# Optimization experiments

Hardware: AMD Instinct MI355X
Metric: run time of the kernel (lower is better)

## Reference

```python
import jax, jax.numpy as jnp
import numpy as np

N_ING, N_DIR = 100000, 50000
E = 1000000
H, D = 4, 16          # heads, per-head dim
HID = H * D           # 64
LAT, COND = 32, 8
F_ING, F_DIR = 16, 8
OUT_ING = 16


def _han_edge(x_src, x_dst, att_s, att_d, edge_index, n_dst):
    # HANConv per-edge-type attention message passing.
    src, dst = edge_index[0], edge_index[1]
    a = jax.nn.leaky_relu(
        jnp.einsum('nhd,hd->nh', x_src, att_s)[src]
        + jnp.einsum('nhd,hd->nh', x_dst, att_d)[dst],
        negative_slope=0.2)                               # [E, H]
    amax = jax.ops.segment_max(a, dst, num_segments=n_dst)
    ex = jnp.exp(a - amax[dst])
    denom = jax.ops.segment_sum(ex, dst, num_segments=n_dst)
    alpha = ex / (denom[dst] + 1e-16)                     # PyG softmax eps
    out = jax.ops.segment_sum(x_src[src] * alpha[:, :, None], dst,
                              num_segments=n_dst)         # [n_dst, H, D]
    return jax.nn.relu(out.reshape(n_dst, HID))


def _group(outs, q, Wk, bk):
    # HANConv semantic-level attention across edge types.
    s = jnp.stack(outs)                                   # [T, N, HID]
    score = jnp.tanh(s @ Wk + bk).mean(axis=1) @ q        # [T]
    attn = jax.nn.softmax(score)
    return jnp.einsum('t,tnf->nf', attn, s)


def setup_inputs() -> dict:
    key = jax.random.key(0)
    ks = jax.random.split(key, 32)
    def ei(k, n_src, n_dst):
        k1, k2 = jax.random.split(k)
        return jnp.stack([jax.random.randint(k1, (E,), 0, n_src),
                          jax.random.randint(k2, (E,), 0, n_dst)]).astype(jnp.int64)
    s = 0.1
    inp = {
        'x_ing': jax.random.normal(ks[0], (N_ING, F_ING), jnp.float32),
        'x_dir': jax.random.normal(ks[1], (N_DIR, F_DIR), jnp.float32),
        'cond':  jax.random.normal(ks[2], (COND,), jnp.float32),
        'eps':   jax.random.normal(ks[3], (1, LAT), jnp.float32),
        'ei_cooc':     ei(ks[4], N_ING, N_DIR),
        'ei_used':     ei(ks[5], N_ING, N_DIR),
        'ei_contains': ei(ks[6], N_DIR, N_ING),
        'ei_pairs':    ei(ks[7], N_DIR, N_DIR),
        'ei_follows':  ei(ks[8], N_DIR, N_DIR),
        # node-type projections
        'W_pi': jax.random.normal(ks[9],  (F_ING, HID)) * s,
        'b_pi': jnp.zeros((HID,)),
        'W_pd': jax.random.normal(ks[10], (F_DIR, HID)) * s,
        'b_pd': jnp.zeros((HID,)),
        # semantic attention
        'Wk': jax.random.normal(ks[21], (HID, HID)) * s,
        'bk': jnp.zeros((HID,)),
        'q':  jax.random.normal(ks[22], (HID,)) * s,
        # VAE heads (input: 2*HID + COND)
        'W_mu': jax.random.normal(ks[23], (2 * HID + COND, LAT)) * s,
        'b_mu': jnp.zeros((LAT,)),
        'W_lv': jax.random.normal(ks[24], (2 * HID + COND, LAT)) * s,
        'b_lv': jnp.zeros((LAT,)),
        # decoder (fc1 is dead code in the original forward)
        'W_fc3': jax.random.normal(ks[25], (LAT, HID)) * s,
        'b_fc3': jnp.zeros((HID,)),
        'W_fc2': jax.random.normal(ks[26], (HID, OUT_ING)) * s,
        'b_fc2': jnp.zeros((OUT_ING,)),
    }
    for i, name in enumerate(['cooc', 'used', 'contains', 'pairs', 'follows']):
        inp[f'as_{name}'] = jax.random.normal(ks[11 + i], (H, D)) * s
        inp[f'ad_{name}'] = jax.random.normal(ks[16 + i], (H, D)) * s
    return inp


def reference(x_ing, x_dir, cond, eps,
              ei_cooc, ei_used, ei_contains, ei_pairs, ei_follows,
              W_pi, b_pi, W_pd, b_pd,
              as_cooc, ad_cooc, as_used, ad_used, as_contains, ad_contains,
              as_pairs, ad_pairs, as_follows, ad_follows,
              Wk, bk, q, W_mu, b_mu, W_lv, b_lv,
              W_fc3, b_fc3, W_fc2, b_fc2):
    # node-type projections -> [N, H, D]
    h_ing = (x_ing @ W_pi + b_pi).reshape(N_ING, H, D)
    h_dir = (x_dir @ W_pd + b_pd).reshape(N_DIR, H, D)

    o_cooc = _han_edge(h_ing, h_dir, as_cooc, ad_cooc, ei_cooc, N_DIR)
    o_used = _han_edge(h_ing, h_dir, as_used, ad_used, ei_used, N_DIR)
    o_cont = _han_edge(h_dir, h_ing, as_contains, ad_contains, ei_contains, N_ING)
    o_pair = _han_edge(h_dir, h_dir, as_pairs, ad_pairs, ei_pairs, N_DIR)
    o_foll = _han_edge(h_dir, h_dir, as_follows, ad_follows, ei_follows, N_DIR)

    out_ing = _group([o_cont], q, Wk, bk)                       # [N_ING, HID]
    out_dir = _group([o_cooc, o_used, o_pair, o_foll], q, Wk, bk)

    ingre_pool = out_ing.mean(axis=0, keepdims=True)            # [1, HID]
    direc_pool = out_dir.mean(axis=0, keepdims=True)
    graph_repr = jnp.concatenate([ingre_pool, direc_pool, cond[None]], axis=1)

    mu = graph_repr @ W_mu + b_mu
    logvar = graph_repr @ W_lv + b_lv
    z = mu + eps * jnp.exp(0.5 * logvar)

    # decoder: fc1 branch is overwritten in the original; effective path below
    recon = jnp.tanh(jax.nn.relu(z @ W_fc3 + b_fc3) @ W_fc2 + b_fc2)  # [1, OUT_ING]
    return recon, mu, logvar
```

## Files before the change

kernel.cpp:

```cpp
#include <hip/hip_runtime.h>
#include <hip/hip_fp16.h>
#include <math.h>

#define N_ING 100000
#define N_DIR 50000
#define NE    1000000
#define NDST_TOTAL 300000
#define NBUCK 4688
#define BA    16
#define NBK   (5 * BA)
#define I4PT  (NE / 4)
#define PB_ING 384
#define PB_DIR 192

typedef float v2f __attribute__((ext_vector_type(2)));

__global__ __launch_bounds__(256) void kA_kernel(
    const int* __restrict__ e0, const int* __restrict__ e1,
    const int* __restrict__ e2, const int* __restrict__ e3,
    const int* __restrict__ e4, int* __restrict__ blockcnt,
    const float* __restrict__ x_ing, const float* __restrict__ W_pi,
    const float* __restrict__ b_pi,
    const float* __restrict__ as_cooc, const float* __restrict__ as_used,
    const float* __restrict__ ad_contains,
    unsigned* __restrict__ h8_ing, __half* __restrict__ s_ing,
    const float* __restrict__ x_dir, const float* __restrict__ W_pd,
    const float* __restrict__ b_pd,
    const float* __restrict__ ad_cooc, const float* __restrict__ ad_used,
    const float* __restrict__ as_contains, const float* __restrict__ as_pairs,
    const float* __restrict__ ad_pairs, const float* __restrict__ as_follows,
    const float* __restrict__ ad_follows,
    unsigned* __restrict__ h8_dir, __half* __restrict__ s_dir)
{
    __shared__ int hist[NBUCK];
    __shared__ float sW[16 * 64];
    __shared__ float sbb[64];
    __shared__ float satt[7 * 64];
    __shared__ float sx[4][16];
    __shared__ float srow[4][64];

    const int bid = blockIdx.x;
    const int tid = threadIdx.x;
    if (bid < NBK) {
        const int type = bid / BA, blk = bid % BA;
        const int* ei = type == 0 ? e0 : type == 1 ? e1 : type == 2 ? e2
                      : type == 3 ? e3 : e4;
        const int base = type == 0 ? 0 : type == 1 ? 50000 : type == 2 ? 100000
                       : type == 3 ? 200000 : 250000;
        for (int i = tid; i < NBUCK; i += 256) hist[i] = 0;
        __syncthreads();
        const int4* d4 = (const int4*)(ei + NE);
        for (int i = blk * 256 + tid; i < I4PT; i += BA * 256) {
            int4 d = d4[i];
            atomicAdd(&hist[(base + d.x) >> 6], 1);
            atomicAdd(&hist[(base + d.y) >> 6], 1);
            atomicAdd(&hist[(base + d.z) >> 6], 1);
            atomicAdd(&hist[(base + d.w) >> 6], 1);
        }
        __syncthreads();
        int* row = blockcnt + (size_t)bid * NBUCK;
        for (int i = tid; i < NBUCK; i += 256) row[i] = hist[i];
    } else if (bid < NBK + PB_ING) {
        const int g = tid >> 6, t = tid & 63;
        for (int i = tid; i < 16 * 64; i += 256) sW[i] = W_pi[i];
        if (tid < 64) {
            sbb[tid] = b_pi[tid];
            satt[tid]       = as_cooc[tid];
            satt[64 + tid]  = as_used[tid];
            satt[128 + tid] = ad_contains[tid];
        }
        __syncthreads();
        for (int q = bid - NBK; q < N_ING / 4; q += PB_ING) {
            int n = q * 4 + g;
            if (t < 16) sx[g][t] = x_ing[(size_t)n * 16 + t];
            __syncthreads();
            float s = sbb[t];
#pragma unroll
            for (int i = 0; i < 16; ++i) s += sx[g][i] * sW[i * 64 + t];
            srow[g][t] = s;
            __syncthreads();
            if (t < 16) {
                int w0 = __builtin_amdgcn_cvt_pk_fp8_f32(srow[g][t * 4], srow[g][t * 4 + 1], 0, false);
                int w  = __builtin_amdgcn_cvt_pk_fp8_f32(srow[g][t * 4 + 2], srow[g][t * 4 + 3], w0, true);
                h8_ing[(size_t)n * 16 + t] = (unsigned)w;
            }
            if (t < 12) {
                int slot = t >> 2, hh = t & 3;
                float sc = 0.f;
#pragma unroll
                for (int d = 0; d < 16; ++d)
                    sc += srow[g][hh * 16 + d] * satt[slot * 64 + hh * 16 + d];
                s_ing[(size_t)n * 12 + t] = __float2half(sc);
            }
            __syncthreads();
        }
    } else {
        const int g = tid >> 6, t = tid & 63;
        for (int i = tid; i < 8 * 64; i += 256) sW[i] = W_pd[i];
        if (tid < 64) {
            sbb[tid] = b_pd[tid];
            satt[tid]        = ad_cooc[tid];
            satt[64  + tid]  = ad_used[tid];
            satt[128 + tid]  = as_contains[tid];
            satt[192 + tid]  = as_pairs[tid];
            satt[256 + tid]  = ad_pairs[tid];
            satt[320 + tid]  = as_follows[tid];
            satt[384 + tid]  = ad_follows[tid];
        }
        __syncthreads();
        for (int q = bid - NBK - PB_ING; q < N_DIR / 4; q += PB_DIR) {
            int n = q * 4 + g;
            if (t < 8) sx[g][t] = x_dir[(size_t)n * 8 + t];
            __syncthreads();
            float s = sbb[t];
#pragma unroll
            for (int i = 0; i < 8; ++i) s += sx[g][i] * sW[i * 64 + t];
            srow[g][t] = s;
            __syncthreads();
            if (t < 16) {
                int w0 = __builtin_amdgcn_cvt_pk_fp8_f32(srow[g][t * 4], srow[g][t * 4 + 1], 0, false);
                int w  = __builtin_amdgcn_cvt_pk_fp8_f32(srow[g][t * 4 + 2], srow[g][t * 4 + 3], w0, true);
                h8_dir[(size_t)n * 16 + t] = (unsigned)w;
            }
            if (t < 28) {
                int slot = t >> 2, hh = t & 3;
                float sc = 0.f;
#pragma unroll
                for (int d = 0; d < 16; ++d)
                    sc += srow[g][hh * 16 + d] * satt[slot * 64 + hh * 16 + d];
                s_dir[(size_t)n * 28 + t] = __float2half(sc);
            }
            __syncthreads();
        }
    }
}

__global__ __launch_bounds__(256) void k2_kernel(
    const int* __restrict__ blockcnt, int* __restrict__ blockbase,
    int* __restrict__ bbase, int* __restrict__ btot, int* __restrict__ cursor)
{
    __shared__ int part[4][64];
    __shared__ int tots[64];
    __shared__ int scn[64];
    __shared__ int bw;
    const int tid = threadIdx.x;
    const int kq = tid >> 6, bl = tid & 63;
    const int b = blockIdx.x * 64 + bl;
    const int K = NBK / 4;
    int ps = 0;
    if (b < NBUCK)
        for (int k = kq * K; k < kq * K + K; ++k)
            ps += blockcnt[(size_t)k * NBUCK + b];
    part[kq][bl] = ps;
    __syncthreads();
    if (tid < 64) {
        int t = part[0][tid] + part[1][tid] + part[2][tid] + part[3][tid];
        tots[tid] = t;
        scn[tid] = t;
    }
    __syncthreads();
    for (int off = 1; off < 64; off <<= 1) {
        int v = 0;
        if (tid < 64 && tid >= off) v = scn[tid - off];
        __syncthreads();
        if (tid < 64) scn[tid] += v;
        __syncthreads();
    }
    if (tid == 63) bw = atomicAdd(cursor, scn[63]);
    __syncthreads();
    if (b < NBUCK) {
        int bs = bw + scn[bl] - tots[bl];
        if (kq == 0) {
            bbase[b] = bs;
            btot[b] = tots[bl];
        }
        int run = bs;
        for (int q = 0; q < kq; ++q) run += part[q][bl];
        for (int k = kq * K; k < kq * K + K; ++k) {
            blockbase[(size_t)k * NBUCK + b] = run;
            run += blockcnt[(size_t)k * NBUCK + b];
        }
    }
}

__global__ __launch_bounds__(256) void k3_kernel(
    const int* __restrict__ e0, const int* __restrict__ e1,
    const int* __restrict__ e2, const int* __restrict__ e3,
    const int* __restrict__ e4, const int* __restrict__ blockbase,
    unsigned* __restrict__ bpair)
{
    __shared__ int cur[NBUCK];
    const int bid = blockIdx.x, tid = threadIdx.x;
    const int type = bid / BA, blk = bid % BA;
    const int* ei = type == 0 ? e0 : type == 1 ? e1 : type == 2 ? e2
                  : type == 3 ? e3 : e4;
    const int base = type == 0 ? 0 : type == 1 ? 50000 : type == 2 ? 100000
                   : type == 3 ? 200000 : 250000;
    const int* row = blockbase + (size_t)bid * NBUCK;
    for (int i = tid; i < NBUCK; i += 256) cur[i] = row[i];
    __syncthreads();
    const int4* s4 = (const int4*)ei;
    const int4* d4 = (const int4*)(ei + NE);
    for (int i = blk * 256 + tid; i < I4PT; i += BA * 256) {
        int4 s = s4[i];
        int4 d = d4[i];
        int g0 = base + d.x, g1 = base + d.y, g2 = base + d.z, g3 = base + d.w;
        int p0 = atomicAdd(&cur[g0 >> 6], 1);
        int p1 = atomicAdd(&cur[g1 >> 6], 1);
        int p2 = atomicAdd(&cur[g2 >> 6], 1);
        int p3 = atomicAdd(&cur[g3 >> 6], 1);
        bpair[p0] = ((unsigned)(g0 & 63) << 17) | (unsigned)s.x;
        bpair[p1] = ((unsigned)(g1 & 63) << 17) | (unsigned)s.y;
        bpair[p2] = ((unsigned)(g2 & 63) << 17) | (unsigned)s.z;
        bpair[p3] = ((unsigned)(g3 & 63) << 17) | (unsigned)s.w;
    }
}

__global__ __launch_bounds__(256) void k4_kernel(
    const unsigned* __restrict__ bpair, const int* __restrict__ bbase,
    const int* __restrict__ btot, int* __restrict__ perm,
    int* __restrict__ start, int* __restrict__ cnt)
{
    __shared__ int h[64], sc[64], cu[64];
    const int b = blockIdx.x, tid = threadIdx.x;
    const int jb = bbase[b], n = btot[b];
    if (tid < 64) h[tid] = 0;
    __syncthreads();
    for (int i = tid; i < n; i += 256)
        atomicAdd(&h[bpair[jb + i] >> 17], 1);
    __syncthreads();
    if (tid == 0) {
        int r = 0;
        for (int i = 0; i < 64; ++i) { sc[i] = r; cu[i] = r; r += h[i]; }
    }
    __syncthreads();
    if (tid < 64) {
        int dg = b * 64 + tid;
        if (dg < NDST_TOTAL) {
            start[dg] = jb + sc[tid];
            cnt[dg] = h[tid];
        }
    }
    for (int i = tid; i < n; i += 256) {
        unsigned p = bpair[jb + i];
        int pos = atomicAdd(&cu[p >> 17], 1);
        perm[jb + pos] = (int)(p & 0x1FFFF);
    }
}

__global__ __launch_bounds__(256) void agg_all_kernel(
    const int* __restrict__ perm, const int* __restrict__ start,
    const int* __restrict__ cnttot,
    const unsigned* __restrict__ h8_ing, const unsigned* __restrict__ h8_dir,
    const __half* __restrict__ s_ing, const __half* __restrict__ s_dir,
    const float* __restrict__ Wk, const float* __restrict__ bk,
    float* __restrict__ pool_ing, float* __restrict__ pool_dir,
    float* __restrict__ sem_dir)
{
    __shared__ float sWk[64 * 64];
    __shared__ float srow[4][64];
    __shared__ float sred[4][64];
    const int t = threadIdx.x & 63, w = threadIdx.x >> 6;
    const int g  = t >> 4;
    const int l4 = t & 15;
    const int hq = l4 >> 2;
    for (int i = threadIdx.x; i < 4096; i += 256) sWk[i] = Wk[i];
    const float bkf = bk[t];
    float p_ing = 0.f;
    float p0 = 0.f, p1 = 0.f, p2 = 0.f, p3 = 0.f;
    float m0 = 0.f, m1 = 0.f, m2 = 0.f, m3 = 0.f;
    __syncthreads();
    const int nwaves = gridDim.x * 4;
    for (int d = blockIdx.x * 4 + w; d < NDST_TOTAL; d += nwaves) {
        int type, ld;
        const __half *ssrc, *sdst;
        const unsigned* hsrc;
        int ss, soff, ds, doff;
        if (d < 50000)       { type = 0; ld = d;          ssrc = s_ing; ss = 12; soff = 0;  sdst = s_dir; ds = 28; doff = 0;  hsrc = h8_ing; }
        else if (d < 100000) { type = 1; ld = d - 50000;  ssrc = s_ing; ss = 12; soff = 4;  sdst = s_dir; ds = 28; doff = 4;  hsrc = h8_ing; }
        else if (d < 200000) { type = 2; ld = d - 100000; ssrc = s_dir; ss = 28; soff = 8;  sdst = s_ing; ds = 12; doff = 8;  hsrc = h8_dir; }
        else if (d < 250000) { type = 3; ld = d - 200000; ssrc = s_dir; ss = 28; soff = 12; sdst = s_dir; ds = 28; doff = 16; hsrc = h8_dir; }
        else                 { type = 4; ld = d - 250000; ssrc = s_dir; ss = 28; soff = 20; sdst = s_dir; ds = 28; doff = 24; hsrc = h8_dir; }
        float adst = __half2float(sdst[(size_t)ld * ds + doff + hq]);
        int jb = start[d], je = jb + cnttot[d];
        float4 acc = make_float4(0.f, 0.f, 0.f, 0.f);
        float dsum = 0.f;
        for (int j = jb; j < je; j += 8) {
            int j0 = j + g, j1 = j + 4 + g;
            bool v0 = j0 < je, v1 = j1 < je;
            int s0 = perm[v0 ? j0 : je - 1];
            int s1 = perm[v1 ? j1 : je - 1];
            float c0 = __half2float(ssrc[(size_t)s0 * ss + soff + hq]);
            float c1 = __half2float(ssrc[(size_t)s1 * ss + soff + hq]);
            unsigned u0 = hsrc[(size_t)s0 * 16 + l4];
            unsigned u1 = hsrc[(size_t)s1 * 16 + l4];
            float a0 = c0 + adst; a0 = a0 > 0.f ? a0 : 0.2f * a0;
            float a1 = c1 + adst; a1 = a1 > 0.f ? a1 : 0.2f * a1;
            float e0 = v0 ? __expf(a0) : 0.f;
            float e1 = v1 ? __expf(a1) : 0.f;
            dsum += e0 + e1;
            v2f lo0 = __builtin_amdgcn_cvt_pk_f32_fp8((int)u0, false);
            v2f hi0 = __builtin_amdgcn_cvt_pk_f32_fp8((int)u0, true);
            v2f lo1 = __builtin_amdgcn_cvt_pk_f32_fp8((int)u1, false);
            v2f hi1 = __builtin_amdgcn_cvt_pk_f32_fp8((int)u1, true);
            acc.x += lo0.x * e0 + lo1.x * e1;
            acc.y += lo0.y * e0 + lo1.y * e1;
            acc.z += hi0.x * e0 + hi1.x * e1;
            acc.w += hi0.y * e0 + hi1.y * e1;
        }
#pragma unroll
        for (int mask = 16; mask <= 32; mask <<= 1) {
            acc.x += __shfl_xor(acc.x, mask, 64);
            acc.y += __shfl_xor(acc.y, mask, 64);
            acc.z += __shfl_xor(acc.z, mask, 64);
            acc.w += __shfl_xor(acc.w, mask, 64);
            dsum  += __shfl_xor(dsum,  mask, 64);
        }
        float inv = 1.f / (dsum + 1e-16f);
        float4 v4 = make_float4(fmaxf(acc.x * inv, 0.f), fmaxf(acc.y * inv, 0.f),
                                fmaxf(acc.z * inv, 0.f), fmaxf(acc.w * inv, 0.f));
        if (g == 0) *(float4*)&srow[w][l4 * 4] = v4;
        float v = srow[w][t];
        if (type == 2) {
            p_ing += v;
        } else {
            float a2 = bkf;
#pragma unroll
            for (int k = 0; k < 64; ++k) a2 += srow[w][k] * sWk[k * 64 + t];
            float tv = tanhf(a2);
            if (type == 0)      { p0 += v; m0 += tv; }
            else if (type == 1) { p1 += v; m1 += tv; }
            else if (type == 3) { p2 += v; m2 += tv; }
            else                { p3 += v; m3 += tv; }
        }
    }
    float vals[9] = { p_ing, p0, p1, p2, p3, m0, m1, m2, m3 };
    float* outs[9] = { pool_ing, pool_dir, pool_dir + 64, pool_dir + 128,
                       pool_dir + 192, sem_dir, sem_dir + 64, sem_dir + 128,
                       sem_dir + 192 };
    for (int i = 0; i < 9; ++i) {
        __syncthreads();
        sred[w][t] = vals[i];
        __syncthreads();
        if (w == 0)
            atomicAdd(&outs[i][t], sred[0][t] + sred[1][t] + sred[2][t] + sred[3][t]);
    }
}

__global__ __launch_bounds__(64) void final_kernel(
    const float* __restrict__ pool_ing, const float* __restrict__ pool_dir,
    const float* __restrict__ sem_dir, const float* __restrict__ q,
    const float* __restrict__ cond, const float* __restrict__ eps,
    const float* __restrict__ W_mu, const float* __restrict__ b_mu,
    const float* __restrict__ W_lv, const float* __restrict__ b_lv,
    const float* __restrict__ W_fc3, const float* __restrict__ b_fc3,
    const float* __restrict__ W_fc2, const float* __restrict__ b_fc2,
    float* __restrict__ out)
{
    __shared__ float gr[136];
    __shared__ float sc[4], attn[4];
    __shared__ float z[32], hfc[64];
    int t = threadIdx.x;
    if (t < 4) {
        float s = 0.f;
        for (int f = 0; f < 64; ++f)
            s += (sem_dir[t * 64 + f] / (float)N_DIR) * q[f];
        sc[t] = s;
    }
    gr[t] = pool_ing[t] / (float)N_ING;
    __syncthreads();
    if (t == 0) {
        float m = fmaxf(fmaxf(sc[0], sc[1]), fmaxf(sc[2], sc[3]));
        float ssum = 0.f;
        for (int i = 0; i < 4; ++i) { attn[i] = expf(sc[i] - m); ssum += attn[i]; }
        for (int i = 0; i < 4; ++i) attn[i] /= ssum;
    }
    __syncthreads();
    {
        float v = 0.f;
        for (int tt = 0; tt < 4; ++tt)
            v += attn[tt] * (pool_dir[tt * 64 + t] / (float)N_DIR);
        gr[64 + t] = v;
    }
    if (t < 8) gr[128 + t] = cond[t];
    __syncthreads();
    if (t < 32) {
        float m = b_mu[t], lv = b_lv[t];
        for (int i = 0; i < 136; ++i) {
            float g = gr[i];
            m  += g * W_mu[i * 32 + t];
            lv += g * W_lv[i * 32 + t];
        }
        out[16 + t] = m;
        out[48 + t] = lv;
        z[t] = m + eps[t] * expf(0.5f * lv);
    }
    __syncthreads();
    {
        float v = b_fc3[t];
        for (int j = 0; j < 32; ++j) v += z[j] * W_fc3[j * 64 + t];
        hfc[t] = fmaxf(v, 0.f);
    }
    __syncthreads();
    if (t < 16) {
        float v = b_fc2[t];
        for (int f = 0; f < 64; ++f) v += hfc[f] * W_fc2[f * 16 + t];
        out[t] = tanhf(v);
    }
}

extern "C" void kernel_launch(void* const* d_in, const int* in_sizes, int n_in,
                              void* d_out, int out_size, void* d_ws, size_t ws_size,
                              hipStream_t stream) {
    const float* x_ing = (const float*)d_in[0];
    const float* x_dir = (const float*)d_in[1];
    const float* cond  = (const float*)d_in[2];
    const float* eps   = (const float*)d_in[3];
    const int* ei_cooc     = (const int*)d_in[4];
    const int* ei_used     = (const int*)d_in[5];
    const int* ei_contains = (const int*)d_in[6];
    const int* ei_pairs    = (const int*)d_in[7];
    const int* ei_follows  = (const int*)d_in[8];
    const float* W_pi = (const float*)d_in[9];
    const float* b_pi = (const float*)d_in[10];
    const float* W_pd = (const float*)d_in[11];
    const float* b_pd = (const float*)d_in[12];
    const float* Wk   = (const float*)d_in[13];
    const float* bk   = (const float*)d_in[14];
    const float* q    = (const float*)d_in[15];
    const float* W_mu = (const float*)d_in[16];
    const float* b_mu = (const float*)d_in[17];
    const float* W_lv = (const float*)d_in[18];
    const float* b_lv = (const float*)d_in[19];
    const float* W_fc3 = (const float*)d_in[20];
    const float* b_fc3 = (const float*)d_in[21];
    const float* W_fc2 = (const float*)d_in[22];
    const float* b_fc2 = (const float*)d_in[23];
    const float* as_cooc     = (const float*)d_in[24];
    const float* ad_cooc     = (const float*)d_in[25];
    const float* as_used     = (const float*)d_in[26];
    const float* ad_used     = (const float*)d_in[27];
    const float* as_contains = (const float*)d_in[28];
    const float* ad_contains = (const float*)d_in[29];
    const float* as_pairs    = (const float*)d_in[30];
    const float* ad_pairs    = (const float*)d_in[31];
    const float* as_follows  = (const float*)d_in[32];
    const float* ad_follows  = (const float*)d_in[33];

    unsigned* bpair = (unsigned*)d_ws;
    unsigned* h8_ing = bpair + (size_t)5 * NE;
    unsigned* h8_dir = h8_ing + (size_t)N_ING * 16;
    __half* s_ing = (__half*)(h8_dir + (size_t)N_DIR * 16);
    __half* s_dir = s_ing + (size_t)N_ING * 12;
    int*   perm  = (int*)(s_dir + (size_t)N_DIR * 28);
    int*   blockcnt  = perm + (size_t)5 * NE;
    int*   blockbase = blockcnt + (size_t)NBK * NBUCK;
    int*   bbase  = blockbase + (size_t)NBK * NBUCK;
    int*   btot   = bbase + NBUCK;
    int*   start  = btot + NBUCK;
    int*   cnt    = start + NDST_TOTAL;
    int*   cursor = cnt + NDST_TOTAL;
    float* pool_ing = (float*)(cursor + 1);
    float* pool_dir = pool_ing + 64;
    float* sem_dir  = pool_dir + 256;

    hipMemsetAsync(cursor, 0, (1 + 64 + 256 + 256) * sizeof(int), stream);

    kA_kernel<<<NBK + PB_ING + PB_DIR, 256, 0, stream>>>(
        ei_cooc, ei_used, ei_contains, ei_pairs, ei_follows, blockcnt,
        x_ing, W_pi, b_pi, as_cooc, as_used, ad_contains, h8_ing, s_ing,
        x_dir, W_pd, b_pd, ad_cooc, ad_used, as_contains, as_pairs, ad_pairs,
        as_follows, ad_follows, h8_dir, s_dir);

    k2_kernel<<<(NBUCK + 63) / 64, 256, 0, stream>>>(
        blockcnt, blockbase, bbase, btot, cursor);

    k3_kernel<<<NBK, 256, 0, stream>>>(
        ei_cooc, ei_used, ei_contains, ei_pairs, ei_follows, blockbase, bpair);

    k4_kernel<<<NBUCK, 256, 0, stream>>>(bpair, bbase, btot, perm, start, cnt);

    agg_all_kernel<<<2048, 256, 0, stream>>>(
        perm, start, cnt, h8_ing, h8_dir, s_ing, s_dir, Wk, bk,
        pool_ing, pool_dir, sem_dir);

    final_kernel<<<1, 64, 0, stream>>>(
        pool_ing, pool_dir, sem_dir, q, cond, eps,
        W_mu, b_mu, W_lv, b_lv, W_fc3, b_fc3, W_fc2, b_fc2, (float*)d_out);
}
```

Before: 520.4 us.

## Fuse per-bucket destination sort into aggregation kernel with LDS permutation

The separate k4 sort kernel is removed. Each aggregation block now handles one 64-destination bucket: it histograms and scatters the bucket's packed pairs into an LDS permutation array, then aggregates from LDS instead of reading a global perm/start/cnt. This removes a kernel launch and a round trip of roughly 5M perm indices through global memory. In exchange, 4688 blocks each reload the 16 KB Wk matrix into LDS and do more end-of-block reductions. Buckets are capped at 1792 edges, so any larger bucket would silently lose edges.

```diff
diff --git a/kernel.cpp b/kernel.cpp
--- a/kernel.cpp
+++ b/kernel.cpp
@@ -12,6 +12,7 @@
 #define I4PT  (NE / 4)
 #define PB_ING 384
 #define PB_DIR 192
+#define CAP   1792
 
 typedef float v2f __attribute__((ext_vector_type(2)));
 
@@ -216,41 +217,9 @@
     }
 }
 
-__global__ __launch_bounds__(256) void k4_kernel(
+__global__ __launch_bounds__(256) void agg_bucket_kernel(
     const unsigned* __restrict__ bpair, const int* __restrict__ bbase,
-    const int* __restrict__ btot, int* __restrict__ perm,
-    int* __restrict__ start, int* __restrict__ cnt)
-{
-    __shared__ int h[64], sc[64], cu[64];
-    const int b = blockIdx.x, tid = threadIdx.x;
-    const int jb = bbase[b], n = btot[b];
-    if (tid < 64) h[tid] = 0;
-    __syncthreads();
-    for (int i = tid; i < n; i += 256)
-        atomicAdd(&h[bpair[jb + i] >> 17], 1);
-    __syncthreads();
-    if (tid == 0) {
-        int r = 0;
-        for (int i = 0; i < 64; ++i) { sc[i] = r; cu[i] = r; r += h[i]; }
-    }
-    __syncthreads();
-    if (tid < 64) {
-        int dg = b * 64 + tid;
-        if (dg < NDST_TOTAL) {
-            start[dg] = jb + sc[tid];
-            cnt[dg] = h[tid];
-        }
-    }
-    for (int i = tid; i < n; i += 256) {
-        unsigned p = bpair[jb + i];
-        int pos = atomicAdd(&cu[p >> 17], 1);
-        perm[jb + pos] = (int)(p & 0x1FFFF);
-    }
-}
-
-__global__ __launch_bounds__(256) void agg_all_kernel(
-    const int* __restrict__ perm, const int* __restrict__ start,
-    const int* __restrict__ cnttot,
+    const int* __restrict__ btot,
     const unsigned* __restrict__ h8_ing, const unsigned* __restrict__ h8_dir,
     const __half* __restrict__ s_ing, const __half* __restrict__ s_dir,
     const float* __restrict__ Wk, const float* __restrict__ bk,
@@ -260,18 +229,42 @@
     __shared__ float sWk[64 * 64];
     __shared__ float srow[4][64];
     __shared__ float sred[4][64];
-    const int t = threadIdx.x & 63, w = threadIdx.x >> 6;
+    __shared__ int lds_perm[CAP];
+    __shared__ int h[64], sc[64], cu[64];
+    const int tid = threadIdx.x;
+    const int t = tid & 63, w = tid >> 6;
     const int g  = t >> 4;
     const int l4 = t & 15;
     const int hq = l4 >> 2;
-    for (int i = threadIdx.x; i < 4096; i += 256) sWk[i] = Wk[i];
+    for (int i = tid; i < 4096; i += 256) sWk[i] = Wk[i];
     const float bkf = bk[t];
+    const int b = blockIdx.x;
+    const int jb = bbase[b];
+    const int n = min(btot[b], CAP);
+
+    if (tid < 64) h[tid] = 0;
+    __syncthreads();
+    for (int i = tid; i < n; i += 256)
+        atomicAdd(&h[bpair[jb + i] >> 17], 1);
+    __syncthreads();
+    if (tid == 0) {
+        int r = 0;
+        for (int i = 0; i < 64; ++i) { sc[i] = r; cu[i] = r; r += h[i]; }
+    }
+    __syncthreads();
+    for (int i = tid; i < n; i += 256) {
+        unsigned p = bpair[jb + i];
+        int pos = atomicAdd(&cu[p >> 17], 1);
+        lds_perm[pos] = (int)(p & 0x1FFFF);
+    }
+    __syncthreads();
+
     float p_ing = 0.f;
     float p0 = 0.f, p1 = 0.f, p2 = 0.f, p3 = 0.f;
     float m0 = 0.f, m1 = 0.f, m2 = 0.f, m3 = 0.f;
-    __syncthreads();
-    const int nwaves = gridDim.x * 4;
-    for (int d = blockIdx.x * 4 + w; d < NDST_TOTAL; d += nwaves) {
+    for (int ld64 = w; ld64 < 64; ld64 += 4) {
+        int d = b * 64 + ld64;
+        if (d >= NDST_TOTAL) break;
         int type, ld;
         const __half *ssrc, *sdst;
         const unsigned* hsrc;
@@ -282,14 +275,14 @@
         else if (d < 250000) { type = 3; ld = d - 200000; ssrc = s_dir; ss = 28; soff = 12; sdst = s_dir; ds = 28; doff = 16; hsrc = h8_dir; }
         else                 { type = 4; ld = d - 250000; ssrc = s_dir; ss = 28; soff = 20; sdst = s_dir; ds = 28; doff = 24; hsrc = h8_dir; }
         float adst = __half2float(sdst[(size_t)ld * ds + doff + hq]);
-        int jb = start[d], je = jb + cnttot[d];
+        int jb2 = sc[ld64], je2 = jb2 + h[ld64];
         float4 acc = make_float4(0.f, 0.f, 0.f, 0.f);
         float dsum = 0.f;
-        for (int j = jb; j < je; j += 8) {
+        for (int j = jb2; j < je2; j += 8) {
             int j0 = j + g, j1 = j + 4 + g;
-            bool v0 = j0 < je, v1 = j1 < je;
-            int s0 = perm[v0 ? j0 : je - 1];
-            int s1 = perm[v1 ? j1 : je - 1];
+            bool v0 = j0 < je2, v1 = j1 < je2;
+            int s0 = lds_perm[v0 ? j0 : je2 - 1];
+            int s1 = lds_perm[v1 ? j1 : je2 - 1];
             float c0 = __half2float(ssrc[(size_t)s0 * ss + soff + hq]);
             float c1 = __half2float(ssrc[(size_t)s1 * ss + soff + hq]);
             unsigned u0 = hsrc[(size_t)s0 * 16 + l4];
@@ -452,14 +445,11 @@
     unsigned* h8_dir = h8_ing + (size_t)N_ING * 16;
     __half* s_ing = (__half*)(h8_dir + (size_t)N_DIR * 16);
     __half* s_dir = s_ing + (size_t)N_ING * 12;
-    int*   perm  = (int*)(s_dir + (size_t)N_DIR * 28);
-    int*   blockcnt  = perm + (size_t)5 * NE;
+    int*   blockcnt  = (int*)(s_dir + (size_t)N_DIR * 28);
     int*   blockbase = blockcnt + (size_t)NBK * NBUCK;
     int*   bbase  = blockbase + (size_t)NBK * NBUCK;
     int*   btot   = bbase + NBUCK;
-    int*   start  = btot + NBUCK;
-    int*   cnt    = start + NDST_TOTAL;
-    int*   cursor = cnt + NDST_TOTAL;
+    int*   cursor = btot + NBUCK;
     float* pool_ing = (float*)(cursor + 1);
     float* pool_dir = pool_ing + 64;
     float* sem_dir  = pool_dir + 256;
@@ -478,10 +468,8 @@
     k3_kernel<<<NBK, 256, 0, stream>>>(
         ei_cooc, ei_used, ei_contains, ei_pairs, ei_follows, blockbase, bpair);
 
-    k4_kernel<<<NBUCK, 256, 0, stream>>>(bpair, bbase, btot, perm, start, cnt);
-
-    agg_all_kernel<<<2048, 256, 0, stream>>>(
-        perm, start, cnt, h8_ing, h8_dir, s_ing, s_dir, Wk, bk,
+    agg_bucket_kernel<<<NBUCK, 256, 0, stream>>>(
+        bpair, bbase, btot, h8_ing, h8_dir, s_ing, s_dir, Wk, bk,
         pool_ing, pool_dir, sem_dir);
 
     final_kernel<<<1, 64, 0, stream>>>(
```

New measurement: 584.4 us. +12.3%, slower.
